# Kernel optimization log

Measured on AMD Instinct MI355X. Metric: run time of the kernel, lower is better.

Reference implementation:

```python
import jax, jax.numpy as jnp
import numpy as np

N_EMBD = 768
N_HEADS = 12
HEAD_DIM = N_EMBD // N_HEADS


def _layernorm(x):
    # LayerNorm without affine params, eps=1e-5 (torch default)
    mu = jnp.mean(x, axis=-1, keepdims=True)
    var = jnp.var(x, axis=-1, keepdims=True)
    return (x - mu) * jax.lax.rsqrt(var + 1e-5)


def setup_inputs() -> dict:
    key = jax.random.key(0)
    ks = jax.random.split(key, 6)
    B, T, C = 1, 4096, N_EMBD
    s = lambda fan_in: 1.0 / np.sqrt(fan_in)
    return {
        "x": jax.random.normal(ks[0], (B, T, C), jnp.float32),
        "W_kqv": jax.random.normal(ks[1], (C, 3 * C), jnp.float32) * s(C),
        "W_proj": jax.random.normal(ks[2], (C, C), jnp.float32) * s(C),
        "W_fc": jax.random.normal(ks[3], (C, 2 * C), jnp.float32) * s(C),
        "b_fc": jax.random.normal(ks[4], (2 * C,), jnp.float32) * s(C),
        "W_cproj": jax.random.normal(ks[5], (2 * C, C), jnp.float32) * s(2 * C),
    }


def _attention(h, W_kqv, W_proj):
    B, T, C = h.shape
    kqv = h @ W_kqv                       # (B, T, 3C)
    kqv = kqv.reshape(B, T, 3, N_HEADS, HEAD_DIM)
    k = kqv[:, :, 0]                      # (B, T, H, Dh) -- note k first, per source
    q = kqv[:, :, 1]
    v = kqv[:, :, 2]
    scale = HEAD_DIM ** -0.5
    scores = jnp.einsum('bqhd,bkhd->bhqk', q, k) * scale
    attn = jax.nn.softmax(scores, axis=-1)
    out = jnp.einsum('bhqk,bkhd->bqhd', attn, v).reshape(B, T, C)
    return out @ W_proj


def _mlp(h, W_fc, b_fc, W_cproj):
    h = h @ W_fc + b_fc
    h = jax.nn.gelu(h, approximate=False)  # torch nn.GELU default = exact erf
    return h @ W_cproj


def reference(x, W_kqv, W_proj, W_fc, b_fc, W_cproj):
    x = x + _attention(_layernorm(x), W_kqv, W_proj)
    x = x + _mlp(_layernorm(x), W_fc, b_fc, W_cproj)
    return x
```

## Files before the change

kernel.cpp:

```cpp
#include <hip/hip_runtime.h>
#include <hip/hip_bf16.h>
#include <math.h>

#define T_SEQ 4096
#define C_EMB 768
#define NHEAD 12
#define HDIM  64
#define NZ    4

typedef __bf16 bf16;
typedef __bf16 bf16x8 __attribute__((ext_vector_type(8)));
typedef __bf16 bf16x4 __attribute__((ext_vector_type(4)));
typedef float  f32x4  __attribute__((ext_vector_type(4)));
typedef float  f32x16 __attribute__((ext_vector_type(16)));

#if __has_builtin(__builtin_amdgcn_exp2f)
#define EXP2 __builtin_amdgcn_exp2f
#else
#define EXP2 exp2f
#endif


__device__ __forceinline__ void stage16(const void* g, void* ldsbase) {
  __builtin_amdgcn_global_load_lds(
      (__attribute__((address_space(1))) const unsigned int*)g,
      (__attribute__((address_space(3))) unsigned int*)ldsbase, 16, 0, 0);
}

__device__ __forceinline__ f32x16 zero16() {
  f32x16 z;
#pragma unroll
  for (int i = 0; i < 16; i++) z[i] = 0.f;
  return z;
}

__device__ __forceinline__ void do_transpose(const float* __restrict__ W,
                                             bf16* __restrict__ Wt, int K, int N,
                                             int bx, int by, int tid,
                                             float (*tile)[33]) {
  const int n0 = bx * 32, k0 = by * 32;
  const int tx = tid & 31, ty = tid >> 5;
#pragma unroll
  for (int i = 0; i < 32; i += 8)
    tile[ty + i][tx] = W[(size_t)(k0 + ty + i) * N + n0 + tx];
  __syncthreads();
#pragma unroll
  for (int i = 0; i < 32; i += 8)
    Wt[(size_t)(n0 + ty + i) * K + k0 + tx] = (bf16)tile[tx][ty + i];
}

__device__ __forceinline__ void do_ln(const float* __restrict__ x,
                                      bf16* __restrict__ y, int row, int t,
                                      float* red) {
  const float* xr = x + (size_t)row * C_EMB;
  float v0 = xr[t], v1 = xr[t + 256], v2 = xr[t + 512];
  float s  = v0 + v1 + v2;
  float ss = v0 * v0 + v1 * v1 + v2 * v2;
#pragma unroll
  for (int m = 1; m < 64; m <<= 1) {
    s += __shfl_xor(s, m);
    ss += __shfl_xor(ss, m);
  }
  const int w = t >> 6;
  if ((t & 63) == 0) { red[w] = s; red[4 + w] = ss; }
  __syncthreads();
  s  = red[0] + red[1] + red[2] + red[3];
  ss = red[4] + red[5] + red[6] + red[7];
  const float mu  = s * (1.0f / C_EMB);
  const float var = ss * (1.0f / C_EMB) - mu * mu;
  const float rs  = rsqrtf(var + 1e-5f);
  bf16* yr = y + (size_t)row * C_EMB;
  yr[t]       = (bf16)((v0 - mu) * rs);
  yr[t + 256] = (bf16)((v1 - mu) * rs);
  yr[t + 512] = (bf16)((v2 - mu) * rs);
}

__global__ void prep(const float* __restrict__ x, bf16* __restrict__ ln_out,
                     const float* __restrict__ W_kqv, bf16* __restrict__ Wkqv_t,
                     const float* __restrict__ W_proj, bf16* __restrict__ Wproj_t,
                     const float* __restrict__ W_fc, bf16* __restrict__ Wfc_t,
                     const float* __restrict__ W_cproj, bf16* __restrict__ Wcp_t) {
  __shared__ float tile[32][33];
  const int b = blockIdx.x, t = threadIdx.x;
  if (b < 1728) {
    do_transpose(W_kqv, Wkqv_t, 768, 2304, b % 72, b / 72, t, tile);
  } else if (b < 2304) {
    const int bb = b - 1728;
    do_transpose(W_proj, Wproj_t, 768, 768, bb % 24, bb / 24, t, tile);
  } else if (b < 3456) {
    const int bb = b - 2304;
    do_transpose(W_fc, Wfc_t, 768, 1536, bb % 48, bb / 48, t, tile);
  } else if (b < 4608) {
    const int bb = b - 3456;
    do_transpose(W_cproj, Wcp_t, 1536, 768, bb % 24, bb / 24, t, tile);
  } else {
    do_ln(x, ln_out, b - 4608, t, &tile[0][0]);
  }
}

__global__ void ln_rows(const float* __restrict__ x, bf16* __restrict__ y) {
  __shared__ float red[8];
  do_ln(x, y, blockIdx.x, threadIdx.x, red);
}

template <int EPI, int BN>
__global__ void gemm_bt(const bf16* __restrict__ A, const bf16* __restrict__ BT,
                        void* __restrict__ Cout, const float* __restrict__ res,
                        const float* __restrict__ bias, int M, int N, int K) {
  __shared__ __align__(16) bf16 As[128 * 64];
  __shared__ __align__(16) bf16 Bs[BN * 64];
  const int nrow = M >> 7;
  const int ncol = N / BN;
  const int rpx = nrow >> 3;
  const int bid = blockIdx.x;
  const int xcd = bid & 7, idx = bid >> 3;
  const int rowb = xcd * rpx + idx / ncol;
  const int colb = idx % ncol;
  const int row0 = rowb * 128, col0 = colb * BN;

  const int tid = threadIdx.x;
  const int w = tid >> 6, lane = tid & 63;
  const int wr = w >> 1, wc = w & 1;
  const int l15 = lane & 15, l4 = lane >> 4;
  constexpr int NF = BN / 32;

  f32x4 acc[4][NF];
#pragma unroll
  for (int m = 0; m < 4; m++)
#pragma unroll
    for (int n = 0; n < NF; n++) acc[m][n] = (f32x4){0.f, 0.f, 0.f, 0.f};

  const int rr = lane >> 3;
  const int c8 = (lane & 7) * 8;

  for (int k0 = 0; k0 < K; k0 += 64) {
    const bf16* gA = A + (size_t)(row0 + w * 32 + rr) * K + k0 + c8;
    const bf16* gB = BT + (size_t)(col0 + w * (BN / 4) + rr) * K + k0 + c8;
#pragma unroll
    for (int i = 0; i < 4; i++)
      stage16(gA + (size_t)(8 * i) * K, As + (w * 32 + 8 * i) * 64);
#pragma unroll
    for (int i = 0; i < BN / 32; i++)
      stage16(gB + (size_t)(8 * i) * K, Bs + (w * (BN / 4) + 8 * i) * 64);
    __syncthreads();

#pragma unroll
    for (int hh = 0; hh < 2; hh++) {
      bf16x8 af[4], bfv[NF];
#pragma unroll
      for (int m = 0; m < 4; m++)
        af[m] = *reinterpret_cast<const bf16x8*>(
            As + (wr * 64 + m * 16 + l15) * 64 + hh * 32 + l4 * 8);
#pragma unroll
      for (int n = 0; n < NF; n++)
        bfv[n] = *reinterpret_cast<const bf16x8*>(
            Bs + (wc * (BN / 2) + n * 16 + l15) * 64 + hh * 32 + l4 * 8);
#pragma unroll
      for (int m = 0; m < 4; m++)
#pragma unroll
        for (int n = 0; n < NF; n++)
          acc[m][n] = __builtin_amdgcn_mfma_f32_16x16x32_bf16(af[m], bfv[n], acc[m][n], 0, 0, 0);
    }
    __syncthreads();
  }

  const int orow = row0 + wr * 64;
  const int ocol = col0 + wc * (BN / 2);
#pragma unroll
  for (int m = 0; m < 4; m++) {
#pragma unroll
    for (int n = 0; n < NF; n++) {
      const int c = ocol + n * 16 + l15;
#pragma unroll
      for (int j = 0; j < 4; j++) {
        const int r = orow + m * 16 + l4 * 4 + j;
        const size_t idx2 = (size_t)r * N + c;
        const float v = acc[m][n][j];
        if (EPI == 0) {
          ((bf16*)Cout)[idx2] = (bf16)v;
        } else if (EPI == 1) {
          ((float*)Cout)[idx2] = res[idx2] + v;
        } else if (EPI == 2) {
          const float h = v + bias[c];
          ((bf16*)Cout)[idx2] = (bf16)(0.5f * h * (1.0f + erff(h * 0.70710678118f)));
        } else if (EPI == 3) {
          ((float*)Cout)[idx2] = res[idx2] + v;
        } else {
          const float sc = (c >= 768 && c < 1536) ? 0.18033688011112042f : 1.0f;
          ((bf16*)Cout)[idx2] = (bf16)(v * sc);
        }
      }
    }
  }
}

__global__ __launch_bounds__(256, 3)
void attn_fused(const bf16* __restrict__ kqv,
                bf16* __restrict__ Opart,
                float* __restrict__ Lpart) {
  const int fid = blockIdx.x;
  const int xs = fid & 7, r = fid >> 3;
  const int qb = r & 31;
  const int s = xs * 6 + (r >> 5);
  const int h = s % 12, z = s / 12;
  const int tid = threadIdx.x, w = tid >> 6, lane = tid & 63;
  const int l31 = lane & 31, hi = lane >> 5;

  __shared__ __align__(16) char KsB[128 * 144];
  __shared__ __align__(16) char VtB[64 * 272];

  const int qrow = qb * 128 + w * 32 + l31;
  const bf16* qp = kqv + (size_t)qrow * 2304 + 768 + h * 64;
  bf16x8 qf[4];
#pragma unroll
  for (int m = 0; m < 4; m++)
    qf[m] = *reinterpret_cast<const bf16x8*>(qp + hi * 8 + 16 * m);

  bf16x8 ones;
#pragma unroll
  for (int e = 0; e < 8; e++) ones[e] = (bf16)1.0f;

  f32x16 accO0 = zero16(), accO1 = zero16(), accL = zero16();

  const int krow = tid >> 1;
  const int kc0 = (tid & 1) * 4;
  const int kb = tid & 31, db = tid >> 5;
  const int lb = ((kb >> 3) & 3) * 32 + ((kb >> 2) & 1) * 16 + (kb & 1) * 8 +
                 ((kb >> 1) & 1) * 4;

  const int kt0 = z * 8;

  bf16x8 kreg[4], vreg[4];
#define LOADKV(kt)                                                               \
  {                                                                              \
    const bf16* kp =                                                             \
        kqv + (size_t)((kt)*128 + krow) * 2304 + h * 64 + kc0 * 8;               \
    _Pragma("unroll") for (int i = 0; i < 4; i++)                                \
        kreg[i] = *reinterpret_cast<const bf16x8*>(kp + i * 8);                  \
    const bf16* vp =                                                             \
        kqv + (size_t)((kt)*128 + kb * 4) * 2304 + 1536 + h * 64 + db * 8;       \
    _Pragma("unroll") for (int r2 = 0; r2 < 4; r2++)                             \
        vreg[r2] = *reinterpret_cast<const bf16x8*>(vp + (size_t)r2 * 2304);     \
  }

  LOADKV(kt0);

  for (int kt = 0; kt < 8; kt++) {
    __syncthreads();
    {
      char* kdst = KsB + krow * 144;
#pragma unroll
      for (int i = 0; i < 4; i++)
        *reinterpret_cast<bf16x8*>(kdst + (kc0 + i) * 16) = kreg[i];
#pragma unroll
      for (int e = 0; e < 8; e++) {
        const int d = db * 8 + e;
        const bf16x4 pk4 = (bf16x4){vreg[0][e], vreg[1][e], vreg[2][e], vreg[3][e]};
        *reinterpret_cast<bf16x4*>(VtB + d * 272 + lb * 2) = pk4;
      }
    }
    __syncthreads();
    if (kt + 1 < 8) LOADKV(kt0 + kt + 1);

    bf16x8 pb[8];
#pragma unroll
    for (int t = 0; t < 4; t++) {
      f32x16 st = zero16();
#pragma unroll
      for (int m = 0; m < 4; m++) {
        const bf16x8 kf = *reinterpret_cast<const bf16x8*>(
            KsB + (size_t)(32 * t + l31) * 144 + (2 * m + hi) * 16);
        st = __builtin_amdgcn_mfma_f32_32x32x16_bf16(kf, qf[m], st, 0, 0, 0);
      }
#pragma unroll
      for (int hf = 0; hf < 2; hf++) {
        bf16x8 p;
#pragma unroll
        for (int j = 0; j < 8; j++) p[j] = (bf16)EXP2(st[hf * 8 + j]);
        pb[2 * t + hf] = p;
      }
    }

#pragma unroll
    for (int mk = 0; mk < 8; mk++) {
      const bf16x8 vf0 = *reinterpret_cast<const bf16x8*>(
          VtB + (size_t)l31 * 272 + (2 * mk + hi) * 16);
      accO0 = __builtin_amdgcn_mfma_f32_32x32x16_bf16(vf0, pb[mk], accO0, 0, 0, 0);
      const bf16x8 vf1 = *reinterpret_cast<const bf16x8*>(
          VtB + (size_t)(32 + l31) * 272 + (2 * mk + hi) * 16);
      accO1 = __builtin_amdgcn_mfma_f32_32x32x16_bf16(vf1, pb[mk], accO1, 0, 0, 0);
      accL = __builtin_amdgcn_mfma_f32_32x32x16_bf16(ones, pb[mk], accL, 0, 0, 0);
    }
  }
#undef LOADKV

  bf16* Oq = Opart + (size_t)z * T_SEQ * C_EMB + (size_t)qrow * C_EMB + h * 64;
#pragma unroll
  for (int s4 = 0; s4 < 4; s4++) {
    const bf16x4 o0 = (bf16x4){(bf16)accO0[4 * s4 + 0], (bf16)accO0[4 * s4 + 1],
                               (bf16)accO0[4 * s4 + 2], (bf16)accO0[4 * s4 + 3]};
    *reinterpret_cast<bf16x4*>(Oq + 8 * s4 + 4 * hi) = o0;
    const bf16x4 o1 = (bf16x4){(bf16)accO1[4 * s4 + 0], (bf16)accO1[4 * s4 + 1],
                               (bf16)accO1[4 * s4 + 2], (bf16)accO1[4 * s4 + 3]};
    *reinterpret_cast<bf16x4*>(Oq + 32 + 8 * s4 + 4 * hi) = o1;
  }
  if (hi == 0)
    Lpart[(size_t)z * NHEAD * T_SEQ + (size_t)h * T_SEQ + qrow] = accL[0];
}

__global__ void attn_combine(const bf16* __restrict__ Opart,
                             const float* __restrict__ Lpart,
                             bf16* __restrict__ out) {
  const int t = threadIdx.x;
  const int rr = t / 96, cc = t % 96;
  const int q = blockIdx.x * 4 + rr;
  const int c = cc * 8;
  const int h = c >> 6;
  float o[8];
#pragma unroll
  for (int j = 0; j < 8; j++) o[j] = 0.f;
  float L = 0.f;
#pragma unroll
  for (int z = 0; z < NZ; z++) {
    const bf16x8 v = *reinterpret_cast<const bf16x8*>(
        Opart + (size_t)z * T_SEQ * C_EMB + (size_t)q * C_EMB + c);
#pragma unroll
    for (int j = 0; j < 8; j++) o[j] += (float)v[j];
    L += Lpart[(size_t)z * NHEAD * T_SEQ + (size_t)h * T_SEQ + q];
  }
  const float inv = 1.0f / L;
  bf16x8 rv;
#pragma unroll
  for (int j = 0; j < 8; j++) rv[j] = (bf16)(o[j] * inv);
  *reinterpret_cast<bf16x8*>(out + (size_t)q * C_EMB + c) = rv;
}

extern "C" void kernel_launch(void* const* d_in, const int* in_sizes, int n_in,
                              void* d_out, int out_size, void* d_ws, size_t ws_size,
                              hipStream_t stream) {
  const float* x       = (const float*)d_in[0];
  const float* W_kqv   = (const float*)d_in[1];
  const float* W_proj  = (const float*)d_in[2];
  const float* W_fc    = (const float*)d_in[3];
  const float* b_fc    = (const float*)d_in[4];
  const float* W_cproj = (const float*)d_in[5];
  float* outp = (float*)d_out;

  char* p = (char*)d_ws;
  bf16* Wkqv_t  = (bf16*)p; p += (size_t)2304 * 768 * 2;
  bf16* Wproj_t = (bf16*)p; p += (size_t)768 * 768 * 2;
  bf16* Wfc_t   = (bf16*)p; p += (size_t)1536 * 768 * 2;
  bf16* Wcp_t   = (bf16*)p; p += (size_t)768 * 1536 * 2;
  bf16* A1      = (bf16*)p; p += (size_t)4096 * 768 * 2;
  bf16* KQV     = (bf16*)p; p += (size_t)4096 * 2304 * 2;
  float* x1     = (float*)p; p += (size_t)4096 * 768 * 4;
  bf16* Opart   = (bf16*)p; p += (size_t)NZ * 4096 * 768 * 2;
  float* Lpart  = (float*)p; p += (size_t)NZ * NHEAD * 4096 * 4;
  bf16* attn_o = A1;
  bf16* A2     = KQV;
  bf16* Hg     = KQV + (size_t)4096 * 768;

  prep<<<8704, 256, 0, stream>>>(x, A1, W_kqv, Wkqv_t, W_proj, Wproj_t,
                                 W_fc, Wfc_t, W_cproj, Wcp_t);
  gemm_bt<4, 64><<<1152, 256, 0, stream>>>(A1, Wkqv_t, KQV, nullptr, nullptr,
                                           4096, 2304, 768);
  attn_fused<<<1536, 256, 0, stream>>>(KQV, Opart, Lpart);
  attn_combine<<<1024, 384, 0, stream>>>(Opart, Lpart, attn_o);
  gemm_bt<1, 64><<<384, 256, 0, stream>>>(attn_o, Wproj_t, x1, x, nullptr,
                                          4096, 768, 768);
  ln_rows<<<4096, 256, 0, stream>>>(x1, A2);
  gemm_bt<2, 64><<<768, 256, 0, stream>>>(A2, Wfc_t, Hg, nullptr, b_fc,
                                          4096, 1536, 768);
  gemm_bt<3, 64><<<384, 256, 0, stream>>>(Hg, Wcp_t, outp, x1, nullptr,
                                          4096, 768, 1536);
}
```

Before: 193.5 us.

## Process two query tiles per wave in attention and sum softmax denominators in registers

Each wave now handles 64 query rows (two 32-row tiles A and B) instead of 32. Every K/V tile staged in shared memory is therefore reused for twice as many queries, and the block count halves. The row-sum of exp values is now accumulated in scalar registers with a cross-half shuffle instead of an extra MFMA against a ones vector. This doubles the accumulator register pressure and drops the launch-bounds occupancy hint, so occupancy may fall.

```diff
diff --git a/kernel.cpp b/kernel.cpp
--- a/kernel.cpp
+++ b/kernel.cpp
@@ -194,14 +194,13 @@
   }
 }
 
-__global__ __launch_bounds__(256, 3)
-void attn_fused(const bf16* __restrict__ kqv,
-                bf16* __restrict__ Opart,
-                float* __restrict__ Lpart) {
+__global__ void attn_fused(const bf16* __restrict__ kqv,
+                           bf16* __restrict__ Opart,
+                           float* __restrict__ Lpart) {
   const int fid = blockIdx.x;
   const int xs = fid & 7, r = fid >> 3;
-  const int qb = r & 31;
-  const int s = xs * 6 + (r >> 5);
+  const int qb = r & 15;
+  const int s = xs * 6 + (r >> 4);
   const int h = s % 12, z = s / 12;
   const int tid = threadIdx.x, w = tid >> 6, lane = tid & 63;
   const int l31 = lane & 31, hi = lane >> 5;
@@ -209,18 +208,20 @@
   __shared__ __align__(16) char KsB[128 * 144];
   __shared__ __align__(16) char VtB[64 * 272];
 
-  const int qrow = qb * 128 + w * 32 + l31;
-  const bf16* qp = kqv + (size_t)qrow * 2304 + 768 + h * 64;
-  bf16x8 qf[4];
-#pragma unroll
-  for (int m = 0; m < 4; m++)
-    qf[m] = *reinterpret_cast<const bf16x8*>(qp + hi * 8 + 16 * m);
-
-  bf16x8 ones;
-#pragma unroll
-  for (int e = 0; e < 8; e++) ones[e] = (bf16)1.0f;
-
-  f32x16 accO0 = zero16(), accO1 = zero16(), accL = zero16();
+  const int qrowA = qb * 256 + w * 64 + l31;
+  const int qrowB = qrowA + 32;
+  const bf16* qpA = kqv + (size_t)qrowA * 2304 + 768 + h * 64;
+  const bf16* qpB = kqv + (size_t)qrowB * 2304 + 768 + h * 64;
+  bf16x8 qfA[4], qfB[4];
+#pragma unroll
+  for (int m = 0; m < 4; m++) {
+    qfA[m] = *reinterpret_cast<const bf16x8*>(qpA + hi * 8 + 16 * m);
+    qfB[m] = *reinterpret_cast<const bf16x8*>(qpB + hi * 8 + 16 * m);
+  }
+
+  f32x16 accOA0 = zero16(), accOA1 = zero16();
+  f32x16 accOB0 = zero16(), accOB1 = zero16();
+  float lsumA = 0.f, lsumB = 0.f;
 
   const int krow = tid >> 1;
   const int kc0 = (tid & 1) * 4;
@@ -262,50 +263,75 @@
     __syncthreads();
     if (kt + 1 < 8) LOADKV(kt0 + kt + 1);
 
-    bf16x8 pb[8];
-#pragma unroll
-    for (int t = 0; t < 4; t++) {
-      f32x16 st = zero16();
-#pragma unroll
-      for (int m = 0; m < 4; m++) {
-        const bf16x8 kf = *reinterpret_cast<const bf16x8*>(
-            KsB + (size_t)(32 * t + l31) * 144 + (2 * m + hi) * 16);
-        st = __builtin_amdgcn_mfma_f32_32x32x16_bf16(kf, qf[m], st, 0, 0, 0);
+#pragma unroll
+    for (int sr = 0; sr < 2; sr++) {
+      bf16x8 pbA[4], pbB[4];
+#pragma unroll
+      for (int t2 = 0; t2 < 2; t2++) {
+        const int tt = 2 * sr + t2;
+        f32x16 stA = zero16(), stB = zero16();
+#pragma unroll
+        for (int m = 0; m < 4; m++) {
+          const bf16x8 kf = *reinterpret_cast<const bf16x8*>(
+              KsB + (size_t)(32 * tt + l31) * 144 + (2 * m + hi) * 16);
+          stA = __builtin_amdgcn_mfma_f32_32x32x16_bf16(kf, qfA[m], stA, 0, 0, 0);
+          stB = __builtin_amdgcn_mfma_f32_32x32x16_bf16(kf, qfB[m], stB, 0, 0, 0);
+        }
+#pragma unroll
+        for (int hf = 0; hf < 2; hf++) {
+          bf16x8 pA, pB;
+#pragma unroll
+          for (int j = 0; j < 8; j++) {
+            const float eA = EXP2(stA[hf * 8 + j]);
+            const float eB = EXP2(stB[hf * 8 + j]);
+            lsumA += eA;
+            lsumB += eB;
+            pA[j] = (bf16)eA;
+            pB[j] = (bf16)eB;
+          }
+          pbA[2 * t2 + hf] = pA;
+          pbB[2 * t2 + hf] = pB;
+        }
       }
 #pragma unroll
-      for (int hf = 0; hf < 2; hf++) {
-        bf16x8 p;
-#pragma unroll
-        for (int j = 0; j < 8; j++) p[j] = (bf16)EXP2(st[hf * 8 + j]);
-        pb[2 * t + hf] = p;
+      for (int mk4 = 0; mk4 < 4; mk4++) {
+        const int mk = 4 * sr + mk4;
+        const bf16x8 vf0 = *reinterpret_cast<const bf16x8*>(
+            VtB + (size_t)l31 * 272 + (2 * mk + hi) * 16);
+        accOA0 = __builtin_amdgcn_mfma_f32_32x32x16_bf16(vf0, pbA[mk4], accOA0, 0, 0, 0);
+        accOB0 = __builtin_amdgcn_mfma_f32_32x32x16_bf16(vf0, pbB[mk4], accOB0, 0, 0, 0);
+        const bf16x8 vf1 = *reinterpret_cast<const bf16x8*>(
+            VtB + (size_t)(32 + l31) * 272 + (2 * mk + hi) * 16);
+        accOA1 = __builtin_amdgcn_mfma_f32_32x32x16_bf16(vf1, pbA[mk4], accOA1, 0, 0, 0);
+        accOB1 = __builtin_amdgcn_mfma_f32_32x32x16_bf16(vf1, pbB[mk4], accOB1, 0, 0, 0);
       }
     }
-
-#pragma unroll
-    for (int mk = 0; mk < 8; mk++) {
-      const bf16x8 vf0 = *reinterpret_cast<const bf16x8*>(
-          VtB + (size_t)l31 * 272 + (2 * mk + hi) * 16);
-      accO0 = __builtin_amdgcn_mfma_f32_32x32x16_bf16(vf0, pb[mk], accO0, 0, 0, 0);
-      const bf16x8 vf1 = *reinterpret_cast<const bf16x8*>(
-          VtB + (size_t)(32 + l31) * 272 + (2 * mk + hi) * 16);
-      accO1 = __builtin_amdgcn_mfma_f32_32x32x16_bf16(vf1, pb[mk], accO1, 0, 0, 0);
-      accL = __builtin_amdgcn_mfma_f32_32x32x16_bf16(ones, pb[mk], accL, 0, 0, 0);
-    }
   }
 #undef LOADKV
 
-  bf16* Oq = Opart + (size_t)z * T_SEQ * C_EMB + (size_t)qrow * C_EMB + h * 64;
+  lsumA += __shfl_xor(lsumA, 32);
+  lsumB += __shfl_xor(lsumB, 32);
+  bf16* OqA = Opart + (size_t)z * T_SEQ * C_EMB + (size_t)qrowA * C_EMB + h * 64;
+  bf16* OqB = Opart + (size_t)z * T_SEQ * C_EMB + (size_t)qrowB * C_EMB + h * 64;
 #pragma unroll
   for (int s4 = 0; s4 < 4; s4++) {
-    const bf16x4 o0 = (bf16x4){(bf16)accO0[4 * s4 + 0], (bf16)accO0[4 * s4 + 1],
-                               (bf16)accO0[4 * s4 + 2], (bf16)accO0[4 * s4 + 3]};
-    *reinterpret_cast<bf16x4*>(Oq + 8 * s4 + 4 * hi) = o0;
-    const bf16x4 o1 = (bf16x4){(bf16)accO1[4 * s4 + 0], (bf16)accO1[4 * s4 + 1],
-                               (bf16)accO1[4 * s4 + 2], (bf16)accO1[4 * s4 + 3]};
-    *reinterpret_cast<bf16x4*>(Oq + 32 + 8 * s4 + 4 * hi) = o1;
-  }
-  if (hi == 0)
-    Lpart[(size_t)z * NHEAD * T_SEQ + (size_t)h * T_SEQ + qrow] = accL[0];
+    *reinterpret_cast<bf16x4*>(OqA + 8 * s4 + 4 * hi) =
+        (bf16x4){(bf16)accOA0[4 * s4 + 0], (bf16)accOA0[4 * s4 + 1],
+                 (bf16)accOA0[4 * s4 + 2], (bf16)accOA0[4 * s4 + 3]};
+    *reinterpret_cast<bf16x4*>(OqA + 32 + 8 * s4 + 4 * hi) =
+        (bf16x4){(bf16)accOA1[4 * s4 + 0], (bf16)accOA1[4 * s4 + 1],
+                 (bf16)accOA1[4 * s4 + 2], (bf16)accOA1[4 * s4 + 3]};
+    *reinterpret_cast<bf16x4*>(OqB + 8 * s4 + 4 * hi) =
+        (bf16x4){(bf16)accOB0[4 * s4 + 0], (bf16)accOB0[4 * s4 + 1],
+                 (bf16)accOB0[4 * s4 + 2], (bf16)accOB0[4 * s4 + 3]};
+    *reinterpret_cast<bf16x4*>(OqB + 32 + 8 * s4 + 4 * hi) =
+        (bf16x4){(bf16)accOB1[4 * s4 + 0], (bf16)accOB1[4 * s4 + 1],
+                 (bf16)accOB1[4 * s4 + 2], (bf16)accOB1[4 * s4 + 3]};
+  }
+  if (hi == 0) {
+    Lpart[(size_t)z * NHEAD * T_SEQ + (size_t)h * T_SEQ + qrowA] = lsumA;
+    Lpart[(size_t)z * NHEAD * T_SEQ + (size_t)h * T_SEQ + qrowB] = lsumB;
+  }
 }
 
 __global__ void attn_combine(const bf16* __restrict__ Opart,
@@ -364,7 +390,7 @@
                                  W_fc, Wfc_t, W_cproj, Wcp_t);
   gemm_bt<4, 64><<<1152, 256, 0, stream>>>(A1, Wkqv_t, KQV, nullptr, nullptr,
                                            4096, 2304, 768);
-  attn_fused<<<1536, 256, 0, stream>>>(KQV, Opart, Lpart);
+  attn_fused<<<768, 256, 0, stream>>>(KQV, Opart, Lpart);
   attn_combine<<<1024, 384, 0, stream>>>(Opart, Lpart, attn_o);
   gemm_bt<1, 64><<<384, 256, 0, stream>>>(attn_o, Wproj_t, x1, x, nullptr,
                                           4096, 768, 768);
```

After: 343.0 us. 77.3% more time.

## Store residual x1 as bf16, use wave-per-row layernorm, raise attention MFMA priority

Applied to the files above, without the earlier changes.

The intermediate residual x1 is now stored in bf16 instead of fp32, which halves its write traffic in the projection epilogue and its read traffic in both the layernorm and the final GEMM epilogue. The layernorm kernel is rewritten to give each wavefront one row, reducing across lanes with shuffles instead of shared memory and using vector loads and stores. The attention compute section is also wrapped in s_setprio so MFMA work gets issue priority over the prefetch loads. The cost is extra rounding error in the residual stream, which feeds straight into the final output.

```diff
diff --git a/kernel.cpp b/kernel.cpp
--- a/kernel.cpp
+++ b/kernel.cpp
@@ -98,14 +98,42 @@
   }
 }
 
-__global__ void ln_rows(const float* __restrict__ x, bf16* __restrict__ y) {
-  __shared__ float red[8];
-  do_ln(x, y, blockIdx.x, threadIdx.x, red);
+__global__ void ln_rows(const bf16* __restrict__ x, bf16* __restrict__ y) {
+  const int w = threadIdx.x >> 6, l = threadIdx.x & 63;
+  const int row = blockIdx.x * 4 + w;
+  const bf16* xr = x + (size_t)row * C_EMB;
+  const bf16x8 v8 = *reinterpret_cast<const bf16x8*>(xr + l * 8);
+  const bf16x4 v4 = *reinterpret_cast<const bf16x4*>(xr + 512 + l * 4);
+  float f[12];
+#pragma unroll
+  for (int j = 0; j < 8; j++) f[j] = (float)v8[j];
+#pragma unroll
+  for (int j = 0; j < 4; j++) f[8 + j] = (float)v4[j];
+  float s = 0.f, ss = 0.f;
+#pragma unroll
+  for (int j = 0; j < 12; j++) { s += f[j]; ss += f[j] * f[j]; }
+#pragma unroll
+  for (int m = 1; m < 64; m <<= 1) {
+    s += __shfl_xor(s, m);
+    ss += __shfl_xor(ss, m);
+  }
+  const float mu  = s * (1.0f / C_EMB);
+  const float var = ss * (1.0f / C_EMB) - mu * mu;
+  const float rs  = rsqrtf(var + 1e-5f);
+  bf16x8 o8;
+  bf16x4 o4;
+#pragma unroll
+  for (int j = 0; j < 8; j++) o8[j] = (bf16)((f[j] - mu) * rs);
+#pragma unroll
+  for (int j = 0; j < 4; j++) o4[j] = (bf16)((f[8 + j] - mu) * rs);
+  bf16* yr = y + (size_t)row * C_EMB;
+  *reinterpret_cast<bf16x8*>(yr + l * 8) = o8;
+  *reinterpret_cast<bf16x4*>(yr + 512 + l * 4) = o4;
 }
 
 template <int EPI, int BN>
 __global__ void gemm_bt(const bf16* __restrict__ A, const bf16* __restrict__ BT,
-                        void* __restrict__ Cout, const float* __restrict__ res,
+                        void* __restrict__ Cout, const void* __restrict__ res,
                         const float* __restrict__ bias, int M, int N, int K) {
   __shared__ __align__(16) bf16 As[128 * 64];
   __shared__ __align__(16) bf16 Bs[BN * 64];
@@ -179,12 +207,12 @@
         if (EPI == 0) {
           ((bf16*)Cout)[idx2] = (bf16)v;
         } else if (EPI == 1) {
-          ((float*)Cout)[idx2] = res[idx2] + v;
+          ((bf16*)Cout)[idx2] = (bf16)(((const float*)res)[idx2] + v);
         } else if (EPI == 2) {
           const float h = v + bias[c];
           ((bf16*)Cout)[idx2] = (bf16)(0.5f * h * (1.0f + erff(h * 0.70710678118f)));
         } else if (EPI == 3) {
-          ((float*)Cout)[idx2] = res[idx2] + v;
+          ((float*)Cout)[idx2] = (float)((const bf16*)res)[idx2] + v;
         } else {
           const float sc = (c >= 768 && c < 1536) ? 0.18033688011112042f : 1.0f;
           ((bf16*)Cout)[idx2] = (bf16)(v * sc);
@@ -262,6 +290,8 @@
     __syncthreads();
     if (kt + 1 < 8) LOADKV(kt0 + kt + 1);
 
+    __builtin_amdgcn_s_setprio(1);
+
     bf16x8 pb[8];
 #pragma unroll
     for (int t = 0; t < 4; t++) {
@@ -291,6 +321,8 @@
       accO1 = __builtin_amdgcn_mfma_f32_32x32x16_bf16(vf1, pb[mk], accO1, 0, 0, 0);
       accL = __builtin_amdgcn_mfma_f32_32x32x16_bf16(ones, pb[mk], accL, 0, 0, 0);
     }
+
+    __builtin_amdgcn_s_setprio(0);
   }
 #undef LOADKV
 
@@ -353,7 +385,7 @@
   bf16* Wcp_t   = (bf16*)p; p += (size_t)768 * 1536 * 2;
   bf16* A1      = (bf16*)p; p += (size_t)4096 * 768 * 2;
   bf16* KQV     = (bf16*)p; p += (size_t)4096 * 2304 * 2;
-  float* x1     = (float*)p; p += (size_t)4096 * 768 * 4;
+  bf16* x1      = (bf16*)p; p += (size_t)4096 * 768 * 2;
   bf16* Opart   = (bf16*)p; p += (size_t)NZ * 4096 * 768 * 2;
   float* Lpart  = (float*)p; p += (size_t)NZ * NHEAD * 4096 * 4;
   bf16* attn_o = A1;
@@ -368,7 +400,7 @@
   attn_combine<<<1024, 384, 0, stream>>>(Opart, Lpart, attn_o);
   gemm_bt<1, 64><<<384, 256, 0, stream>>>(attn_o, Wproj_t, x1, x, nullptr,
                                           4096, 768, 768);
-  ln_rows<<<4096, 256, 0, stream>>>(x1, A2);
+  ln_rows<<<1024, 256, 0, stream>>>(x1, A2);
   gemm_bt<2, 64><<<768, 256, 0, stream>>>(A2, Wfc_t, Hg, nullptr, b_fc,
                                           4096, 1536, 768);
   gemm_bt<3, 64><<<384, 256, 0, stream>>>(Hg, Wcp_t, outp, x1, nullptr,
```

Measured after the change: 189.9 us. No clear change (-1.9%).
